# Kernel optimization log

Measured on AMD Instinct MI355X. Metric: run time of the kernel, lower is better.

## Reference

```python
import jax, jax.numpy as jnp
import numpy as np

N_NODES = 100000
N_EDGES = 3200000
DIMS = [1, 64, 32, 16, 1]  # GCNConv channel sizes from __init__


def _add_self_loops(edge_index, n):
    loop = jnp.arange(n, dtype=edge_index.dtype)
    src = jnp.concatenate([edge_index[0], loop])
    dst = jnp.concatenate([edge_index[1], loop])
    return src, dst


def _deg_inv_sqrt(dst, n):
    # symmetric GCN norm: deg over destination nodes of A + I (edge_weight = 1)
    deg = jax.ops.segment_sum(jnp.ones_like(dst, dtype=jnp.float32), dst, num_segments=n)
    return jnp.where(deg > 0, jax.lax.rsqrt(deg), 0.0)


def _gcn_conv(x, src, dst, dinv, W, b, n):
    h = x @ W                                   # [N, out] transform first (PyG order)
    coef = dinv[src] * dinv[dst]                # [E+N] edge normalization
    out = jax.ops.segment_sum(coef[:, None] * h[src], dst, num_segments=n)
    return out + b


def setup_inputs() -> dict:
    key = jax.random.key(0)
    ks = jax.random.split(key, 12)
    x = jax.random.normal(ks[0], (N_NODES, DIMS[0]), dtype=jnp.float32)
    edge_index = jax.random.randint(ks[1], (2, N_EDGES), 0, N_NODES, dtype=jnp.int64)
    params = {}
    for i in range(4):
        fin, fout = DIMS[i], DIMS[i + 1]
        scale = 1.0 / np.sqrt(fin)
        params[f"W{i+1}"] = jax.random.uniform(ks[2 + 2 * i], (fin, fout), jnp.float32, -scale, scale)
        params[f"b{i+1}"] = jnp.zeros((fout,), jnp.float32)
    return {"x": x, "edge_index": edge_index, **params}


def reference(x, edge_index, W1, b1, W2, b2, W3, b3, W4, b4):
    n = x.shape[0]
    src, dst = _add_self_loops(edge_index, n)
    dinv = _deg_inv_sqrt(dst, n)
    h = jax.nn.relu(_gcn_conv(x, src, dst, dinv, W1, b1, n))
    h = jax.nn.relu(_gcn_conv(h, src, dst, dinv, W2, b2, n))
    h = jax.nn.relu(_gcn_conv(h, src, dst, dinv, W3, b3, n))
    h = _gcn_conv(h, src, dst, dinv, W4, b4, n)
    return h
```

## Files before the change

### kernel.cpp

```cpp
#include <hip/hip_runtime.h>

#define NPB_SHIFT 8
#define NPB 256
#define EPB 6144
#define MAXB 512
#define BCAP 9216
#define SRC_BITS 17
#define SRC_MASK 0x1FFFFu

__global__ void bcur_init_kernel(unsigned int* __restrict__ bcur, int NB) {
    int b = blockIdx.x * blockDim.x + threadIdx.x;
    if (b < NB) bcur[b] = (unsigned int)b * BCAP;
}

__global__ __launch_bounds__(256) void partition_kernel(const int* __restrict__ src,
                                                        const int* __restrict__ dst,
                                                        unsigned int* __restrict__ bcur,
                                                        unsigned int* __restrict__ staged, int E, int NB) {
    __shared__ unsigned int hist[MAXB], sc[MAXB], lbase[MAXB], lcur[MAXB], gbase[MAXB];
    __shared__ unsigned int stage[EPB];
    __shared__ unsigned short sbuck[EPB];
    int start = blockIdx.x * EPB;
    int cnt = min(EPB, E - start);
    for (int j = threadIdx.x; j < MAXB; j += 256) hist[j] = 0u;
    __syncthreads();
    for (int k = threadIdx.x; k < cnt; k += 256)
        atomicAdd(&hist[((unsigned int)dst[start + k]) >> NPB_SHIFT], 1u);
    __syncthreads();
    {
        int i0 = threadIdx.x, i1 = threadIdx.x + 256;
        sc[i0] = hist[i0]; sc[i1] = hist[i1];
        __syncthreads();
        for (int o = 1; o < MAXB; o <<= 1) {
            unsigned int v0 = (i0 >= o) ? sc[i0 - o] : 0u;
            unsigned int v1 = (i1 >= o) ? sc[i1 - o] : 0u;
            __syncthreads();
            sc[i0] += v0; sc[i1] += v1;
            __syncthreads();
        }
    }
    for (int j = threadIdx.x; j < MAXB; j += 256) {
        unsigned int c = hist[j];
        unsigned int ex = sc[j] - c;
        lbase[j] = ex; lcur[j] = ex;
        gbase[j] = (j < NB && c) ? atomicAdd(&bcur[j], c) : 0u;
    }
    __syncthreads();
    for (int k = threadIdx.x; k < cnt; k += 256) {
        unsigned int d = (unsigned int)dst[start + k];
        unsigned int b = d >> NPB_SHIFT;
        unsigned int pos = atomicAdd(&lcur[b], 1u);
        stage[pos] = ((d & (NPB - 1)) << SRC_BITS) | (unsigned int)src[start + k];
        sbuck[pos] = (unsigned short)b;
    }
    __syncthreads();
    for (int t = threadIdx.x; t < cnt; t += 256) {
        unsigned int b = sbuck[t];
        staged[(size_t)gbase[b] + (t - lbase[b])] = stage[t];
    }
}

__global__ __launch_bounds__(256) void build_csr_kernel(const unsigned int* __restrict__ staged,
                                                        const unsigned int* __restrict__ bcur,
                                                        const float* __restrict__ x,
                                                        unsigned int* __restrict__ csr,
                                                        unsigned int* __restrict__ off,
                                                        unsigned int* __restrict__ deg,
                                                        float* __restrict__ dinv,
                                                        float* __restrict__ ttx, int N) {
    __shared__ unsigned int cnt[NPB], loff[NPB], ncur[NPB];
    int b = blockIdx.x;
    unsigned int base = (unsigned int)b * BCAP;
    unsigned int m = bcur[b] - base;
    int node0 = b << NPB_SHIFT;
    cnt[threadIdx.x] = 0u;
    __syncthreads();
    for (unsigned int t = threadIdx.x; t < m; t += 256)
        atomicAdd(&cnt[staged[(size_t)base + t] >> SRC_BITS], 1u);
    __syncthreads();
    unsigned int v = cnt[threadIdx.x];
    loff[threadIdx.x] = v;
    __syncthreads();
    for (int o = 1; o < NPB; o <<= 1) {
        unsigned int a = (threadIdx.x >= (unsigned)o) ? loff[threadIdx.x - o] : 0u;
        __syncthreads();
        loff[threadIdx.x] += a;
        __syncthreads();
    }
    unsigned int ex = loff[threadIdx.x] - v;
    ncur[threadIdx.x] = ex;
    int node = node0 + threadIdx.x;
    if (node < N) {
        off[node] = base + ex;
        deg[node] = v;
        float di = 1.0f / sqrtf((float)(v + 1u));
        dinv[node] = di;
        ttx[node] = di * x[node];
    }
    __syncthreads();
    for (unsigned int t = threadIdx.x; t < m; t += 256) {
        unsigned int rec = staged[(size_t)base + t];
        unsigned int p = atomicAdd(&ncur[rec >> SRC_BITS], 1u);
        csr[(size_t)base + p] = rec & SRC_MASK;
    }
}

__global__ __launch_bounds__(256) void lut_kernel(const float* __restrict__ W1, const float* __restrict__ b1,
                                                  const float* __restrict__ W2,
                                                  float* __restrict__ Alut, float* __restrict__ Blut,
                                                  float* __restrict__ tvals) {
    __shared__ float w1[64], bb[64], tv[64];
    __shared__ int rnk[64];
    __shared__ float sW2[64 * 32];
    __shared__ double red[2][256];
    int tid = threadIdx.x;
    if (tid < 64) {
        float w = W1[tid], b = b1[tid];
        w1[tid] = w; bb[tid] = b;
        tv[tid] = (w != 0.f) ? (-b / w) : __uint_as_float(0x7F800000u);
    }
    for (int t = tid; t < 64 * 32; t += 256) sW2[t] = W2[t];
    __syncthreads();
    if (tid < 64) {
        int r = 0;
        float tj = tv[tid];
        for (int k = 0; k < 64; ++k)
            if (w1[k] != 0.f && (tv[k] < tj || (tv[k] == tj && k < tid))) ++r;
        rnk[tid] = r;
        if (blockIdx.x == 0) tvals[tid] = tv[tid];
    }
    __syncthreads();
    int s = blockIdx.x;
    int c = tid & 31, slice = tid >> 5;
    double da = 0.0, db = 0.0;
#pragma unroll
    for (int u = 0; u < 8; ++u) {
        int j = slice * 8 + u;
        float w = w1[j];
        bool act = (w > 0.f) ? (rnk[j] < s) : ((w < 0.f) ? (rnk[j] >= s) : (bb[j] > 0.f));
        if (act) {
            double w2 = (double)sW2[j * 32 + c];
            da += (double)w * w2;
            db += (double)bb[j] * w2;
        }
    }
    red[0][tid] = da; red[1][tid] = db;
    __syncthreads();
    for (int o = 128; o >= 32; o >>= 1) {
        if (tid < o) { red[0][tid] += red[0][tid + o]; red[1][tid] += red[1][tid + o]; }
        __syncthreads();
    }
    if (tid < 32) {
        Alut[s * 32 + tid] = (float)red[0][tid];
        Blut[s * 32 + tid] = (float)red[1][tid];
    }
}

__global__ __launch_bounds__(256) void gather1_kernel(const unsigned int* __restrict__ csr,
                                                      const unsigned int* __restrict__ off,
                                                      const unsigned int* __restrict__ deg,
                                                      const float* __restrict__ dinv,
                                                      const float* __restrict__ tt,
                                                      const float* __restrict__ tvals,
                                                      uint4* __restrict__ recs, int N) {
    __shared__ float st[64];
    for (int t = threadIdx.x; t < 64; t += 256) st[t] = tvals[t];
    __syncthreads();
    int tid = blockIdx.x * 256 + threadIdx.x;
    int i = tid >> 2, l = tid & 3;
    if (i >= N) return;
    unsigned int o = off[i], n = deg[i];
    float acc0 = 0.f, acc1 = 0.f;
    unsigned int k = l;
    for (; k + 4 < n; k += 8) { acc0 += tt[csr[o + k]]; acc1 += tt[csr[o + k + 4]]; }
    if (k < n) acc0 += tt[csr[o + k]];
    float acc = acc0 + acc1;
    acc += __shfl_xor(acc, 1, 4);
    acc += __shfl_xor(acc, 2, 4);
    float di = dinv[i];
    float a = di * (acc + tt[i]);
    unsigned int cv = 0;
#pragma unroll
    for (int j = 0; j < 16; ++j) cv += (st[l * 16 + j] < a) ? 1u : 0u;
    cv += __shfl_xor(cv, 1, 4);
    cv += __shfl_xor(cv, 2, 4);
    if (l == 0) recs[i] = make_uint4(__float_as_uint(a * di), __float_as_uint(di), cv, 0u);
}

#define G2_NODES 64
#define FMA_REC(R, AX, AY)                                                   \
    {                                                                        \
        float4 A_ = sAB[(R).z * 16 + c];                                     \
        float p_ = __uint_as_float((R).x), q_ = __uint_as_float((R).y);      \
        (AX).x = fmaf(A_.x, p_, fmaf(A_.z, q_, (AX).x));                     \
        (AX).y = fmaf(A_.y, p_, fmaf(A_.w, q_, (AX).y));                     \
        (void)(AY);                                                          \
    }
__global__ __launch_bounds__(256) void gather2t3_kernel(const unsigned int* __restrict__ csr,
                                                        const unsigned int* __restrict__ off,
                                                        const unsigned int* __restrict__ deg,
                                                        const float* __restrict__ dinv,
                                                        const uint4* __restrict__ recs,
                                                        const float* __restrict__ Alut, const float* __restrict__ Blut,
                                                        const float* __restrict__ b2, const float* __restrict__ W3,
                                                        float* __restrict__ tt3, int N) {
    __shared__ float4 sAB[65 * 16];
    __shared__ float sW3[32 * 16];
    __shared__ float sb2[32];
    for (int t = threadIdx.x; t < 65 * 16; t += 256) {
        int s = t >> 4, cc = t & 15;
        sAB[t] = make_float4(Alut[s * 32 + cc], Alut[s * 32 + cc + 16],
                             Blut[s * 32 + cc], Blut[s * 32 + cc + 16]);
    }
    for (int t = threadIdx.x; t < 32 * 16; t += 256) sW3[t] = W3[t];
    if (threadIdx.x < 32) sb2[threadIdx.x] = b2[threadIdx.x];
    __syncthreads();

    int g = threadIdx.x >> 4, c = threadIdx.x & 15;
    for (int iter = 0; iter < 4; ++iter) {
        int d = blockIdx.x * G2_NODES + iter * 16 + g;
        if (d >= N) continue;
        float dd = dinv[d];
        unsigned int o = off[d], n = deg[d];
        uint4 rs = recs[d];
        float ps = __uint_as_float(rs.x), qs = __uint_as_float(rs.y);
        float4 ABs = sAB[rs.z * 16 + c];
        float2 a0 = make_float2(fmaf(ABs.x, ps, ABs.z * qs), fmaf(ABs.y, ps, ABs.w * qs));
        float2 a1 = make_float2(0.f, 0.f);
        unsigned int P = n >> 1;
        if (P >= 2) {
            unsigned int c0 = csr[o], c1 = csr[o + 1];
            unsigned int c2 = csr[o + 2], c3 = csr[o + 3];
            uint4 r0 = recs[c0], r1 = recs[c1];
            for (unsigned int j = 0; j + 2 < P; ++j) {
                unsigned int base = o + 2 * j;
                unsigned int nc0 = csr[base + 4], nc1 = csr[base + 5];
                uint4 nr0 = recs[c2], nr1 = recs[c3];
                {
                    float4 A0 = sAB[r0.z * 16 + c], A1 = sAB[r1.z * 16 + c];
                    float p0 = __uint_as_float(r0.x), q0 = __uint_as_float(r0.y);
                    float p1 = __uint_as_float(r1.x), q1 = __uint_as_float(r1.y);
                    a0.x = fmaf(A0.x, p0, fmaf(A0.z, q0, a0.x));
                    a0.y = fmaf(A0.y, p0, fmaf(A0.w, q0, a0.y));
                    a1.x = fmaf(A1.x, p1, fmaf(A1.z, q1, a1.x));
                    a1.y = fmaf(A1.y, p1, fmaf(A1.w, q1, a1.y));
                }
                r0 = nr0; r1 = nr1; c2 = nc0; c3 = nc1;
            }
            uint4 m0 = recs[c2], m1 = recs[c3];
            {
                float4 A0 = sAB[r0.z * 16 + c], A1 = sAB[r1.z * 16 + c];
                float p0 = __uint_as_float(r0.x), q0 = __uint_as_float(r0.y);
                float p1 = __uint_as_float(r1.x), q1 = __uint_as_float(r1.y);
                a0.x = fmaf(A0.x, p0, fmaf(A0.z, q0, a0.x));
                a0.y = fmaf(A0.y, p0, fmaf(A0.w, q0, a0.y));
                a1.x = fmaf(A1.x, p1, fmaf(A1.z, q1, a1.x));
                a1.y = fmaf(A1.y, p1, fmaf(A1.w, q1, a1.y));
            }
            {
                float4 A0 = sAB[m0.z * 16 + c], A1 = sAB[m1.z * 16 + c];
                float p0 = __uint_as_float(m0.x), q0 = __uint_as_float(m0.y);
                float p1 = __uint_as_float(m1.x), q1 = __uint_as_float(m1.y);
                a0.x = fmaf(A0.x, p0, fmaf(A0.z, q0, a0.x));
                a0.y = fmaf(A0.y, p0, fmaf(A0.w, q0, a0.y));
                a1.x = fmaf(A1.x, p1, fmaf(A1.z, q1, a1.x));
                a1.y = fmaf(A1.y, p1, fmaf(A1.w, q1, a1.y));
            }
        } else if (P == 1) {
            uint4 r0 = recs[csr[o]], r1 = recs[csr[o + 1]];
            float4 A0 = sAB[r0.z * 16 + c], A1 = sAB[r1.z * 16 + c];
            float p0 = __uint_as_float(r0.x), q0 = __uint_as_float(r0.y);
            float p1 = __uint_as_float(r1.x), q1 = __uint_as_float(r1.y);
            a0.x = fmaf(A0.x, p0, fmaf(A0.z, q0, a0.x));
            a0.y = fmaf(A0.y, p0, fmaf(A0.w, q0, a0.y));
            a1.x = fmaf(A1.x, p1, fmaf(A1.z, q1, a1.x));
            a1.y = fmaf(A1.y, p1, fmaf(A1.w, q1, a1.y));
        }
        if (n & 1u) {
            uint4 r0 = recs[csr[o + n - 1]];
            float4 A0 = sAB[r0.z * 16 + c];
            float p0 = __uint_as_float(r0.x), q0 = __uint_as_float(r0.y);
            a0.x = fmaf(A0.x, p0, fmaf(A0.z, q0, a0.x));
            a0.y = fmaf(A0.y, p0, fmaf(A0.w, q0, a0.y));
        }
        float hx = fmaxf(fmaf(dd, a0.x + a1.x, sb2[c]), 0.f);
        float hy = fmaxf(fmaf(dd, a0.y + a1.y, sb2[c + 16]), 0.f);

        float t3 = 0.f;
#pragma unroll
        for (int kk = 0; kk < 16; ++kk) {
            float hk = __shfl(hx, kk, 16);
            t3 = fmaf(hk, sW3[kk * 16 + c], t3);
        }
#pragma unroll
        for (int kk = 0; kk < 16; ++kk) {
            float hk = __shfl(hy, kk, 16);
            t3 = fmaf(hk, sW3[(kk + 16) * 16 + c], t3);
        }
        tt3[(size_t)d * 16 + c] = dd * t3;
    }
}

__global__ __launch_bounds__(256) void gather3t4_kernel(const unsigned int* __restrict__ csr,
                                                        const unsigned int* __restrict__ off,
                                                        const unsigned int* __restrict__ deg,
                                                        const float* __restrict__ dinv,
                                                        const float* __restrict__ tt3,
                                                        const float* __restrict__ b3, const float* __restrict__ W4,
                                                        float* __restrict__ tt4, int N) {
    int tid = blockIdx.x * 256 + threadIdx.x;
    int d = tid >> 2, l = tid & 3;
    if (d >= N) return;
    float dd = dinv[d];
    unsigned int o = off[d], n = deg[d];
    const float4* t34 = reinterpret_cast<const float4*>(tt3);
    float4 acc = t34[(size_t)d * 4 + l];
    float4 acc1 = make_float4(0.f, 0.f, 0.f, 0.f);
    unsigned int k = 0;
    if (n >= 4) {
        unsigned int s0 = csr[o], s1 = csr[o + 1], s2 = csr[o + 2], s3 = csr[o + 3];
        k = 4;
        for (; k + 3 < n; k += 4) {
            unsigned int t0 = csr[o + k], t1 = csr[o + k + 1], t2 = csr[o + k + 2], t3 = csr[o + k + 3];
            float4 v0 = t34[(size_t)s0 * 4 + l];
            float4 v1 = t34[(size_t)s1 * 4 + l];
            float4 v2 = t34[(size_t)s2 * 4 + l];
            float4 v3 = t34[(size_t)s3 * 4 + l];
            acc.x += v0.x + v2.x; acc.y += v0.y + v2.y; acc.z += v0.z + v2.z; acc.w += v0.w + v2.w;
            acc1.x += v1.x + v3.x; acc1.y += v1.y + v3.y; acc1.z += v1.z + v3.z; acc1.w += v1.w + v3.w;
            s0 = t0; s1 = t1; s2 = t2; s3 = t3;
        }
        {
            float4 v0 = t34[(size_t)s0 * 4 + l];
            float4 v1 = t34[(size_t)s1 * 4 + l];
            float4 v2 = t34[(size_t)s2 * 4 + l];
            float4 v3 = t34[(size_t)s3 * 4 + l];
            acc.x += v0.x + v2.x; acc.y += v0.y + v2.y; acc.z += v0.z + v2.z; acc.w += v0.w + v2.w;
            acc1.x += v1.x + v3.x; acc1.y += v1.y + v3.y; acc1.z += v1.z + v3.z; acc1.w += v1.w + v3.w;
        }
    }
    for (; k < n; ++k) {
        float4 v0 = t34[(size_t)csr[o + k] * 4 + l];
        acc.x += v0.x; acc.y += v0.y; acc.z += v0.z; acc.w += v0.w;
    }
    acc.x += acc1.x; acc.y += acc1.y; acc.z += acc1.z; acc.w += acc1.w;
    float4 b3v = reinterpret_cast<const float4*>(b3)[l];
    float4 w4v = reinterpret_cast<const float4*>(W4)[l];
    float v = fmaxf(fmaf(dd, acc.x, b3v.x), 0.f) * w4v.x;
    v = fmaf(fmaxf(fmaf(dd, acc.y, b3v.y), 0.f), w4v.y, v);
    v = fmaf(fmaxf(fmaf(dd, acc.z, b3v.z), 0.f), w4v.z, v);
    v = fmaf(fmaxf(fmaf(dd, acc.w, b3v.w), 0.f), w4v.w, v);
    v += __shfl_xor(v, 1, 4);
    v += __shfl_xor(v, 2, 4);
    if (l == 0) tt4[d] = dd * v;
}

__global__ void gather4_kernel(const unsigned int* __restrict__ csr, const unsigned int* __restrict__ off,
                               const unsigned int* __restrict__ deg, const float* __restrict__ dinv,
                               const float* __restrict__ tt, const float* __restrict__ b4,
                               float* __restrict__ out, int N) {
    int tid = blockIdx.x * blockDim.x + threadIdx.x;
    int i = tid >> 2, l = tid & 3;
    if (i >= N) return;
    unsigned int o = off[i], n = deg[i];
    float acc0 = 0.f, acc1 = 0.f;
    unsigned int k = l;
    for (; k + 4 < n; k += 8) { acc0 += tt[csr[o + k]]; acc1 += tt[csr[o + k + 4]]; }
    if (k < n) acc0 += tt[csr[o + k]];
    float acc = acc0 + acc1;
    acc += __shfl_xor(acc, 1, 4);
    acc += __shfl_xor(acc, 2, 4);
    if (l == 0) out[i] = dinv[i] * (acc + tt[i]) + b4[0];
}

extern "C" void kernel_launch(void* const* d_in, const int* in_sizes, int n_in,
                              void* d_out, int out_size, void* d_ws, size_t ws_size,
                              hipStream_t stream) {
    const float* x  = (const float*)d_in[0];
    const int* eidx = (const int*)d_in[1];
    const float* W1 = (const float*)d_in[2];
    const float* b1 = (const float*)d_in[3];
    const float* W2 = (const float*)d_in[4];
    const float* b2 = (const float*)d_in[5];
    const float* W3 = (const float*)d_in[6];
    const float* b3 = (const float*)d_in[7];
    const float* W4 = (const float*)d_in[8];
    const float* b4 = (const float*)d_in[9];
    float* out = (float*)d_out;

    const int N = in_sizes[0];
    const int E = in_sizes[1] / 2;
    const int* src = eidx;
    const int* dst = eidx + E;
    const int NB = (N + NPB - 1) >> NPB_SHIFT;

    char* ws = (char*)d_ws;
    unsigned int* bcur  = (unsigned int*)ws;  ws += MAXB * 4;
    float* tvals = (float*)ws;                ws += 64 * 4;
    float* Alut  = (float*)ws;                ws += 65 * 32 * 4;
    float* Blut  = (float*)ws;                ws += 65 * 32 * 4;
    unsigned int* off = (unsigned int*)ws;    ws += (size_t)N * 4;
    unsigned int* deg = (unsigned int*)ws;    ws += (size_t)N * 4;
    float* dinv = (float*)ws;                 ws += (size_t)N * 4;
    float* ttx  = (float*)ws;                 ws += (size_t)N * 4;
    float* tt4  = (float*)ws;                 ws += (size_t)N * 4;
    uint4* recs = (uint4*)ws;                 ws += (size_t)N * 16;
    unsigned int* csr = (unsigned int*)ws;    ws += (size_t)NB * BCAP * 4;
    unsigned int* staged = (unsigned int*)ws;
    float* tt3 = (float*)staged;

    const int nPartBlocks = (E + EPB - 1) / EPB;

    bcur_init_kernel<<<(NB + 255) / 256, 256, 0, stream>>>(bcur, NB);
    partition_kernel<<<nPartBlocks, 256, 0, stream>>>(src, dst, bcur, staged, E, NB);
    build_csr_kernel<<<NB, 256, 0, stream>>>(staged, bcur, x, csr, off, deg, dinv, ttx, N);
    lut_kernel<<<65, 256, 0, stream>>>(W1, b1, W2, Alut, Blut, tvals);

    gather1_kernel<<<((size_t)N * 4 + 255) / 256, 256, 0, stream>>>(csr, off, deg, dinv, ttx, tvals, recs, N);
    gather2t3_kernel<<<(N + G2_NODES - 1) / G2_NODES, 256, 0, stream>>>(csr, off, deg, dinv, recs, Alut, Blut, b2, W3, tt3, N);
    gather3t4_kernel<<<((size_t)N * 4 + 255) / 256, 256, 0, stream>>>(csr, off, deg, dinv, tt3, b3, W4, tt4, N);
    gather4_kernel<<<((size_t)N * 4 + 255) / 256, 256, 0, stream>>>(csr, off, deg, dinv, tt4, b4, out, N);
}
```

Before: 209.2 us.

## Use 8 lanes per node in layer-2 gather and fold bcur init into LUT kernel

The layer-2 gather/transform kernel now assigns 8 threads per node instead of 16. Each thread accumulates 4 of the 32 channels and produces 2 of the 16 outputs of the W3 transform, with LUT and W3 shared tables re-laid out to match. This halves the redundant per-node record loads (csr/recs) across lanes and doubles nodes per block, at the cost of more registers and LDS reads per thread. Separately, the bucket-cursor init is merged into the LUT kernel, which is launched first, removing one kernel launch.

```diff
diff --git a/kernel.cpp b/kernel.cpp
--- a/kernel.cpp
+++ b/kernel.cpp
@@ -7,11 +7,6 @@
 #define BCAP 9216
 #define SRC_BITS 17
 #define SRC_MASK 0x1FFFFu
-
-__global__ void bcur_init_kernel(unsigned int* __restrict__ bcur, int NB) {
-    int b = blockIdx.x * blockDim.x + threadIdx.x;
-    if (b < NB) bcur[b] = (unsigned int)b * BCAP;
-}
 
 __global__ __launch_bounds__(256) void partition_kernel(const int* __restrict__ src,
                                                         const int* __restrict__ dst,
@@ -108,12 +103,16 @@
 __global__ __launch_bounds__(256) void lut_kernel(const float* __restrict__ W1, const float* __restrict__ b1,
                                                   const float* __restrict__ W2,
                                                   float* __restrict__ Alut, float* __restrict__ Blut,
-                                                  float* __restrict__ tvals) {
+                                                  float* __restrict__ tvals,
+                                                  unsigned int* __restrict__ bcur, int NB) {
     __shared__ float w1[64], bb[64], tv[64];
     __shared__ int rnk[64];
     __shared__ float sW2[64 * 32];
     __shared__ double red[2][256];
     int tid = threadIdx.x;
+    if (blockIdx.x == 0) {
+        for (int t = tid; t < NB; t += 256) bcur[t] = (unsigned int)t * BCAP;
+    }
     if (tid < 64) {
         float w = W1[tid], b = b1[tid];
         w1[tid] = w; bb[tid] = b;
@@ -187,14 +186,15 @@
     if (l == 0) recs[i] = make_uint4(__float_as_uint(a * di), __float_as_uint(di), cv, 0u);
 }
 
-#define G2_NODES 64
-#define FMA_REC(R, AX, AY)                                                   \
-    {                                                                        \
-        float4 A_ = sAB[(R).z * 16 + c];                                     \
-        float p_ = __uint_as_float((R).x), q_ = __uint_as_float((R).y);      \
-        (AX).x = fmaf(A_.x, p_, fmaf(A_.z, q_, (AX).x));                     \
-        (AX).y = fmaf(A_.y, p_, fmaf(A_.w, q_, (AX).y));                     \
-        (void)(AY);                                                          \
+#define G2_ITERS 4
+#define FMA4(R, ACC)                                                          \
+    {                                                                         \
+        float4 A_ = sA2[(R).z * 8 + cc], B_ = sB2[(R).z * 8 + cc];            \
+        float p_ = __uint_as_float((R).x), q_ = __uint_as_float((R).y);       \
+        (ACC).x = fmaf(A_.x, p_, fmaf(B_.x, q_, (ACC).x));                    \
+        (ACC).y = fmaf(A_.y, p_, fmaf(B_.y, q_, (ACC).y));                    \
+        (ACC).z = fmaf(A_.z, p_, fmaf(B_.z, q_, (ACC).z));                    \
+        (ACC).w = fmaf(A_.w, p_, fmaf(B_.w, q_, (ACC).w));                    \
     }
 __global__ __launch_bounds__(256) void gather2t3_kernel(const unsigned int* __restrict__ csr,
                                                         const unsigned int* __restrict__ off,
@@ -204,29 +204,36 @@
                                                         const float* __restrict__ Alut, const float* __restrict__ Blut,
                                                         const float* __restrict__ b2, const float* __restrict__ W3,
                                                         float* __restrict__ tt3, int N) {
-    __shared__ float4 sAB[65 * 16];
-    __shared__ float sW3[32 * 16];
+    __shared__ float4 sA2[65 * 8], sB2[65 * 8];
+    __shared__ float2 sW3p[32 * 8];
     __shared__ float sb2[32];
-    for (int t = threadIdx.x; t < 65 * 16; t += 256) {
-        int s = t >> 4, cc = t & 15;
-        sAB[t] = make_float4(Alut[s * 32 + cc], Alut[s * 32 + cc + 16],
-                             Blut[s * 32 + cc], Blut[s * 32 + cc + 16]);
-    }
-    for (int t = threadIdx.x; t < 32 * 16; t += 256) sW3[t] = W3[t];
+    for (int t = threadIdx.x; t < 65 * 8; t += 256) {
+        int s = t >> 3, q = t & 7;
+        sA2[t] = make_float4(Alut[s * 32 + q], Alut[s * 32 + q + 8],
+                             Alut[s * 32 + q + 16], Alut[s * 32 + q + 24]);
+        sB2[t] = make_float4(Blut[s * 32 + q], Blut[s * 32 + q + 8],
+                             Blut[s * 32 + q + 16], Blut[s * 32 + q + 24]);
+    }
+    for (int t = threadIdx.x; t < 32 * 8; t += 256) {
+        int k = t >> 3, q = t & 7;
+        sW3p[t] = make_float2(W3[k * 16 + q], W3[k * 16 + q + 8]);
+    }
     if (threadIdx.x < 32) sb2[threadIdx.x] = b2[threadIdx.x];
     __syncthreads();
 
-    int g = threadIdx.x >> 4, c = threadIdx.x & 15;
-    for (int iter = 0; iter < 4; ++iter) {
-        int d = blockIdx.x * G2_NODES + iter * 16 + g;
+    int g = threadIdx.x >> 3, cc = threadIdx.x & 7;
+    for (int iter = 0; iter < G2_ITERS; ++iter) {
+        int d = blockIdx.x * (32 * G2_ITERS) + iter * 32 + g;
         if (d >= N) continue;
         float dd = dinv[d];
         unsigned int o = off[d], n = deg[d];
         uint4 rs = recs[d];
         float ps = __uint_as_float(rs.x), qs = __uint_as_float(rs.y);
-        float4 ABs = sAB[rs.z * 16 + c];
-        float2 a0 = make_float2(fmaf(ABs.x, ps, ABs.z * qs), fmaf(ABs.y, ps, ABs.w * qs));
-        float2 a1 = make_float2(0.f, 0.f);
+        float4 As = sA2[rs.z * 8 + cc], Bs = sB2[rs.z * 8 + cc];
+        float4 aP, aQ;
+        aP.x = fmaf(As.x, ps, Bs.x * qs); aP.y = fmaf(As.y, ps, Bs.y * qs);
+        aP.z = fmaf(As.z, ps, Bs.z * qs); aP.w = fmaf(As.w, ps, Bs.w * qs);
+        aQ = make_float4(0.f, 0.f, 0.f, 0.f);
         unsigned int P = n >> 1;
         if (P >= 2) {
             unsigned int c0 = csr[o], c1 = csr[o + 1];
@@ -236,68 +243,52 @@
                 unsigned int base = o + 2 * j;
                 unsigned int nc0 = csr[base + 4], nc1 = csr[base + 5];
                 uint4 nr0 = recs[c2], nr1 = recs[c3];
-                {
-                    float4 A0 = sAB[r0.z * 16 + c], A1 = sAB[r1.z * 16 + c];
-                    float p0 = __uint_as_float(r0.x), q0 = __uint_as_float(r0.y);
-                    float p1 = __uint_as_float(r1.x), q1 = __uint_as_float(r1.y);
-                    a0.x = fmaf(A0.x, p0, fmaf(A0.z, q0, a0.x));
-                    a0.y = fmaf(A0.y, p0, fmaf(A0.w, q0, a0.y));
-                    a1.x = fmaf(A1.x, p1, fmaf(A1.z, q1, a1.x));
-                    a1.y = fmaf(A1.y, p1, fmaf(A1.w, q1, a1.y));
-                }
+                FMA4(r0, aP); FMA4(r1, aQ);
                 r0 = nr0; r1 = nr1; c2 = nc0; c3 = nc1;
             }
             uint4 m0 = recs[c2], m1 = recs[c3];
-            {
-                float4 A0 = sAB[r0.z * 16 + c], A1 = sAB[r1.z * 16 + c];
-                float p0 = __uint_as_float(r0.x), q0 = __uint_as_float(r0.y);
-                float p1 = __uint_as_float(r1.x), q1 = __uint_as_float(r1.y);
-                a0.x = fmaf(A0.x, p0, fmaf(A0.z, q0, a0.x));
-                a0.y = fmaf(A0.y, p0, fmaf(A0.w, q0, a0.y));
-                a1.x = fmaf(A1.x, p1, fmaf(A1.z, q1, a1.x));
-                a1.y = fmaf(A1.y, p1, fmaf(A1.w, q1, a1.y));
-            }
-            {
-                float4 A0 = sAB[m0.z * 16 + c], A1 = sAB[m1.z * 16 + c];
-                float p0 = __uint_as_float(m0.x), q0 = __uint_as_float(m0.y);
-                float p1 = __uint_as_float(m1.x), q1 = __uint_as_float(m1.y);
-                a0.x = fmaf(A0.x, p0, fmaf(A0.z, q0, a0.x));
-                a0.y = fmaf(A0.y, p0, fmaf(A0.w, q0, a0.y));
-                a1.x = fmaf(A1.x, p1, fmaf(A1.z, q1, a1.x));
-                a1.y = fmaf(A1.y, p1, fmaf(A1.w, q1, a1.y));
-            }
+            FMA4(r0, aP); FMA4(r1, aQ);
+            FMA4(m0, aP); FMA4(m1, aQ);
         } else if (P == 1) {
             uint4 r0 = recs[csr[o]], r1 = recs[csr[o + 1]];
-            float4 A0 = sAB[r0.z * 16 + c], A1 = sAB[r1.z * 16 + c];
-            float p0 = __uint_as_float(r0.x), q0 = __uint_as_float(r0.y);
-            float p1 = __uint_as_float(r1.x), q1 = __uint_as_float(r1.y);
-            a0.x = fmaf(A0.x, p0, fmaf(A0.z, q0, a0.x));
-            a0.y = fmaf(A0.y, p0, fmaf(A0.w, q0, a0.y));
-            a1.x = fmaf(A1.x, p1, fmaf(A1.z, q1, a1.x));
-            a1.y = fmaf(A1.y, p1, fmaf(A1.w, q1, a1.y));
+            FMA4(r0, aP); FMA4(r1, aQ);
         }
         if (n & 1u) {
             uint4 r0 = recs[csr[o + n - 1]];
-            float4 A0 = sAB[r0.z * 16 + c];
-            float p0 = __uint_as_float(r0.x), q0 = __uint_as_float(r0.y);
-            a0.x = fmaf(A0.x, p0, fmaf(A0.z, q0, a0.x));
-            a0.y = fmaf(A0.y, p0, fmaf(A0.w, q0, a0.y));
-        }
-        float hx = fmaxf(fmaf(dd, a0.x + a1.x, sb2[c]), 0.f);
-        float hy = fmaxf(fmaf(dd, a0.y + a1.y, sb2[c + 16]), 0.f);
-
-        float t3 = 0.f;
-#pragma unroll
-        for (int kk = 0; kk < 16; ++kk) {
-            float hk = __shfl(hx, kk, 16);
-            t3 = fmaf(hk, sW3[kk * 16 + c], t3);
-        }
-#pragma unroll
-        for (int kk = 0; kk < 16; ++kk) {
-            float hk = __shfl(hy, kk, 16);
-            t3 = fmaf(hk, sW3[(kk + 16) * 16 + c], t3);
-        }
-        tt3[(size_t)d * 16 + c] = dd * t3;
+            FMA4(r0, aP);
+        }
+        float hv0 = fmaxf(fmaf(dd, aP.x + aQ.x, sb2[cc]), 0.f);
+        float hv1 = fmaxf(fmaf(dd, aP.y + aQ.y, sb2[cc + 8]), 0.f);
+        float hv2 = fmaxf(fmaf(dd, aP.z + aQ.z, sb2[cc + 16]), 0.f);
+        float hv3 = fmaxf(fmaf(dd, aP.w + aQ.w, sb2[cc + 24]), 0.f);
+
+        float t0 = 0.f, t1 = 0.f;
+#pragma unroll
+        for (int l2 = 0; l2 < 8; ++l2) {
+            float hk = __shfl(hv0, l2, 8);
+            float2 w = sW3p[l2 * 8 + cc];
+            t0 = fmaf(hk, w.x, t0); t1 = fmaf(hk, w.y, t1);
+        }
+#pragma unroll
+        for (int l2 = 0; l2 < 8; ++l2) {
+            float hk = __shfl(hv1, l2, 8);
+            float2 w = sW3p[(8 + l2) * 8 + cc];
+            t0 = fmaf(hk, w.x, t0); t1 = fmaf(hk, w.y, t1);
+        }
+#pragma unroll
+        for (int l2 = 0; l2 < 8; ++l2) {
+            float hk = __shfl(hv2, l2, 8);
+            float2 w = sW3p[(16 + l2) * 8 + cc];
+            t0 = fmaf(hk, w.x, t0); t1 = fmaf(hk, w.y, t1);
+        }
+#pragma unroll
+        for (int l2 = 0; l2 < 8; ++l2) {
+            float hk = __shfl(hv3, l2, 8);
+            float2 w = sW3p[(24 + l2) * 8 + cc];
+            t0 = fmaf(hk, w.x, t0); t1 = fmaf(hk, w.y, t1);
+        }
+        tt3[(size_t)d * 16 + cc] = dd * t0;
+        tt3[(size_t)d * 16 + cc + 8] = dd * t1;
     }
 }
 
@@ -411,13 +402,12 @@
 
     const int nPartBlocks = (E + EPB - 1) / EPB;
 
-    bcur_init_kernel<<<(NB + 255) / 256, 256, 0, stream>>>(bcur, NB);
+    lut_kernel<<<65, 256, 0, stream>>>(W1, b1, W2, Alut, Blut, tvals, bcur, NB);
     partition_kernel<<<nPartBlocks, 256, 0, stream>>>(src, dst, bcur, staged, E, NB);
     build_csr_kernel<<<NB, 256, 0, stream>>>(staged, bcur, x, csr, off, deg, dinv, ttx, N);
-    lut_kernel<<<65, 256, 0, stream>>>(W1, b1, W2, Alut, Blut, tvals);
 
     gather1_kernel<<<((size_t)N * 4 + 255) / 256, 256, 0, stream>>>(csr, off, deg, dinv, ttx, tvals, recs, N);
-    gather2t3_kernel<<<(N + G2_NODES - 1) / G2_NODES, 256, 0, stream>>>(csr, off, deg, dinv, recs, Alut, Blut, b2, W3, tt3, N);
+    gather2t3_kernel<<<(N + 32 * G2_ITERS - 1) / (32 * G2_ITERS), 256, 0, stream>>>(csr, off, deg, dinv, recs, Alut, Blut, b2, W3, tt3, N);
     gather3t4_kernel<<<((size_t)N * 4 + 255) / 256, 256, 0, stream>>>(csr, off, deg, dinv, tt3, b3, W4, tt4, N);
     gather4_kernel<<<((size_t)N * 4 + 255) / 256, 256, 0, stream>>>(csr, off, deg, dinv, tt4, b4, out, N);
 }
```

After: 194.1 us. -7.2%, faster.
